# Performance work log

Measured on AMD Instinct MI355X. Metric: run time of the kernel, lower is better.

Reference implementation:

```python
import jax, jax.numpy as jnp
import numpy as np

N = 50000   # nodes
E = 800000  # edges
F = 64      # node_feature_dim
H = 128     # hidden_dim


def setup_inputs() -> dict:
    key = jax.random.key(0)
    ks = jax.random.split(key, 20)
    def w(k, shape, fan_in):
        return jax.random.normal(k, shape, jnp.float32) / np.sqrt(fan_in)
    return {
        "x": jax.random.normal(ks[0], (N, F), jnp.float32),
        "edge_index": jax.random.randint(ks[1], (2, E), 0, N, jnp.int32),
        "enc_w1": w(ks[2], (F, H), F), "enc_b1": jnp.zeros((H,), jnp.float32),
        "enc_w2": w(ks[3], (H, H), H), "enc_b2": jnp.zeros((H,), jnp.float32),
        "w_c1": w(ks[4], (H, H), H), "b_c1": jnp.zeros((H,), jnp.float32),
        "w_c2": w(ks[5], (H, H), H), "b_c2": jnp.zeros((H,), jnp.float32),
        "w_c3": w(ks[6], (H, H), H), "b_c3": jnp.zeros((H,), jnp.float32),
        "dec_w1": w(ks[7], (H, H), H), "dec_b1": jnp.zeros((H,), jnp.float32),
        "dec_w2": w(ks[8], (H, F), H), "dec_b2": jnp.zeros((F,), jnp.float32),
    }


def _gcn_conv(h, W, b, src, dst, dinv):
    # PyG GCNConv: D^-1/2 (A+I) D^-1/2 (h W) + b  (self-loops already in src/dst)
    hw = h @ W                                   # [N, H]
    norm = dinv[src] * dinv[dst]                 # [E+N]
    msg = hw[src] * norm[:, None]                # gather + scale
    return jax.ops.segment_sum(msg, dst, num_segments=N) + b


def reference(x, edge_index, enc_w1, enc_b1, enc_w2, enc_b2,
              w_c1, b_c1, w_c2, b_c2, w_c3, b_c3,
              dec_w1, dec_b1, dec_w2, dec_b2):
    loop = jnp.arange(N, dtype=edge_index.dtype)
    src = jnp.concatenate([edge_index[0], loop])
    dst = jnp.concatenate([edge_index[1], loop])
    deg = jax.ops.segment_sum(jnp.ones_like(dst, jnp.float32), dst, num_segments=N)
    dinv = jax.lax.rsqrt(deg)  # deg >= 1 because of self-loops

    h = jax.nn.relu(x @ enc_w1 + enc_b1) @ enc_w2 + enc_b2  # encoder MLP
    h = jax.nn.relu(_gcn_conv(h, w_c1, b_c1, src, dst, dinv))
    h = jax.nn.relu(_gcn_conv(h, w_c2, b_c2, src, dst, dinv))
    h = jax.nn.relu(_gcn_conv(h, w_c3, b_c3, src, dst, dinv))
    # window_size == 1: chunk+cat is identity
    out = jax.nn.relu(h @ dec_w1 + dec_b1) @ dec_w2 + dec_b2  # decoder MLP
    return jax.nn.sigmoid(out)
```

## Files before the change

kernel.cpp:

```cpp
#include <hip/hip_runtime.h>
#include <stdint.h>

#define NN 50000
#define NE 800000
#define FD 64
#define HD 128
#define NBKT 196
#define BCAP 5120
#define P1E 8192

typedef __attribute__((ext_vector_type(8))) short short8;
typedef __attribute__((ext_vector_type(4))) float f32x4;

#define AS1 __attribute__((address_space(1)))
#define AS3 __attribute__((address_space(3)))

__device__ __forceinline__ float bflo(unsigned int v) {
    union { unsigned int u; float f; } c; c.u = v << 16; return c.f;
}
__device__ __forceinline__ float bfhi(unsigned int v) {
    union { unsigned int u; float f; } c; c.u = v & 0xffff0000u; return c.f;
}
__device__ __forceinline__ unsigned short f2bf(float f) {
    union { float f; unsigned int u; } c; c.f = f;
    unsigned int u = c.u;
    return (unsigned short)((u + 0x7fffu + ((u >> 16) & 1u)) >> 16);
}
__device__ __forceinline__ unsigned int pack2(float a, float b) {
    return (unsigned int)f2bf(a) | ((unsigned int)f2bf(b) << 16);
}

__global__ void wt0_k(const float* __restrict__ w0, unsigned short* __restrict__ t0) {
    int e = blockIdx.x * 256 + threadIdx.x;
    int k = e >> 7, c = e & 127;
    int gsw = (k >> 3) ^ (c & 7);
    t0[c * 64 + gsw * 8 + (k & 7)] = f2bf(w0[e]);
}

template <int K, int COLS, int EPI, bool BIAS, bool RSCALE, bool A_F32, bool OUT_F32>
__device__ __forceinline__ void mgemm_dev(
    int bid,
    const void* __restrict__ Av,
    const unsigned short* __restrict__ Wt,
    const float* __restrict__ bias,
    const float* __restrict__ dinv,
    void* __restrict__ outv, int nrows)
{
    constexpr int NB = COLS / 16;
    constexpr int KC = K / 32;
    constexpr int GMASK = (K >> 3) - 1;
    __shared__ __align__(16) unsigned char Ws8[COLS * K * 2];

    const int tid = threadIdx.x;
    const int wave = tid >> 6;
    const int lane = tid & 63;

    {
        constexpr int ROUNDS = COLS * K * 2 / 4096;
        const int gb = wave * 1024 + lane * 16;
        const int lb = wave * 1024;
        #pragma unroll
        for (int r = 0; r < ROUNDS; r++) {
            __builtin_amdgcn_global_load_lds(
                (const AS1 unsigned int*)((const unsigned char*)Wt + r * 4096 + gb),
                (AS3 unsigned int*)(Ws8 + r * 4096 + lb),
                16, 0, 0);
        }
    }

    const int m = lane & 15;
    const int q = lane >> 4;
    const int row0 = bid * 64 + wave * 16;

    f32x4 acc[NB];
    #pragma unroll
    for (int i = 0; i < NB; i++) acc[i] = (f32x4){0.f, 0.f, 0.f, 0.f};

    const bool arow_ok = !A_F32 || (row0 + m) < nrows;

    short8 af[KC];
    #pragma unroll
    for (int kc = 0; kc < KC; kc++) {
        if constexpr (A_F32) {
            const float* arowf = (const float*)Av + (size_t)(row0 + m) * K + q * 8 + kc * 32;
            float4 lo = make_float4(0.f, 0.f, 0.f, 0.f), hi = lo;
            if (arow_ok) { lo = *(const float4*)arowf; hi = *(const float4*)(arowf + 4); }
            af[kc][0] = (short)f2bf(lo.x); af[kc][1] = (short)f2bf(lo.y);
            af[kc][2] = (short)f2bf(lo.z); af[kc][3] = (short)f2bf(lo.w);
            af[kc][4] = (short)f2bf(hi.x); af[kc][5] = (short)f2bf(hi.y);
            af[kc][6] = (short)f2bf(hi.z); af[kc][7] = (short)f2bf(hi.w);
        } else {
            const unsigned short* arow = (const unsigned short*)Av + (size_t)(row0 + m) * K + q * 8 + kc * 32;
            af[kc] = *(const short8*)arow;
        }
    }
    __syncthreads();

    #pragma unroll
    for (int kc = 0; kc < KC; kc++) {
        #pragma unroll
        for (int nb = 0; nb < NB; nb++) {
            const int c = nb * 16 + m;
            const int gsw = (kc * 4 + q) ^ (c & GMASK);
            short8 bf = *(const short8*)&Ws8[(c * K + gsw * 8) * 2];
            acc[nb] = __builtin_amdgcn_mfma_f32_16x16x32_bf16(af[kc], bf, acc[nb], 0, 0, 0);
        }
    }

    float bv[NB];
    #pragma unroll
    for (int nb = 0; nb < NB; nb++) bv[nb] = BIAS ? bias[nb * 16 + m] : 0.f;

    #pragma unroll
    for (int r = 0; r < 4; r++) {
        int row = row0 + q * 4 + r;
        if (row < nrows) {
            float sc = RSCALE ? dinv[row] : 1.f;
            #pragma unroll
            for (int nb = 0; nb < NB; nb++) {
                float t = acc[nb][r];
                if (RSCALE) t *= sc;
                t += bv[nb];
                if (EPI == 1) t = fmaxf(t, 0.f);
                if (EPI == 2) t = 1.f / (1.f + __expf(-t));
                if constexpr (OUT_F32) {
                    ((float*)outv)[(size_t)row * COLS + nb * 16 + m] = t;
                } else {
                    ((unsigned short*)outv)[(size_t)row * COLS + nb * 16 + m] = f2bf(t);
                }
            }
        }
    }
}

template <int K, int COLS, int EPI, bool BIAS, bool RSCALE, bool A_F32, bool OUT_F32>
__global__ __launch_bounds__(256) void mgemm_k(
    const void* __restrict__ Av, const unsigned short* __restrict__ Wt,
    const float* __restrict__ bias, const float* __restrict__ dinv,
    void* __restrict__ outv, int nrows)
{
    mgemm_dev<K, COLS, EPI, BIAS, RSCALE, A_F32, OUT_F32>(blockIdx.x, Av, Wt, bias, dinv, outv, nrows);
}

__global__ __launch_bounds__(256) void k1_k(
    const float* __restrict__ x, const unsigned short* __restrict__ t0s,
    const float* __restrict__ enc_b1, unsigned short* __restrict__ bufA,
    const int* __restrict__ src, const int* __restrict__ dst,
    int* __restrict__ gcnt, unsigned int* __restrict__ bucket,
    const float* __restrict__ w1, const float* __restrict__ w2,
    const float* __restrict__ w3, const float* __restrict__ w4,
    const float* __restrict__ w5, const float* __restrict__ w6,
    unsigned short* __restrict__ t1, unsigned short* __restrict__ t2,
    unsigned short* __restrict__ t3, unsigned short* __restrict__ t4,
    unsigned short* __restrict__ t5, unsigned short* __restrict__ t6,
    int gb, int pb)
{
    const int b = blockIdx.x;
    if (b < gb) {
        mgemm_dev<64, 128, 1, true, false, true, false>(b, x, t0s, enc_b1, nullptr, bufA, NN);
    } else if (b < gb + pb) {
        __shared__ int lcnt[256], lsw[256], lexc[256], lofs[256], lrank[256];
        __shared__ unsigned int stage[P1E];
        const int tid = threadIdx.x;
        const int bb = b - gb;
        lcnt[tid] = 0; lrank[tid] = 0;
        __syncthreads();
        unsigned int ent[P1E / 256];
        #pragma unroll
        for (int u = 0; u < P1E / 256; u++) {
            int g = bb * P1E + u * 256 + tid;
            if (g < NE) {
                int d = dst[g], s = src[g];
                int bk = d >> 8;
                atomicAdd(&lcnt[bk], 1);
                ent[u] = (unsigned int)s | ((unsigned int)(d & 255) << 16)
                       | ((unsigned int)bk << 24);
            } else ent[u] = 0xFFFFFFFFu;
        }
        __syncthreads();
        int v = lcnt[tid];
        lsw[tid] = v; __syncthreads();
        for (int d = 1; d < 256; d <<= 1) {
            int xx = (tid >= d) ? lsw[tid - d] : 0; __syncthreads();
            lsw[tid] += xx; __syncthreads();
        }
        lexc[tid] = lsw[tid] - v;
        lofs[tid] = (v > 0) ? atomicAdd(&gcnt[tid], v) : 0;
        __syncthreads();
        #pragma unroll
        for (int u = 0; u < P1E / 256; u++) {
            if (ent[u] != 0xFFFFFFFFu) {
                int bk = ent[u] >> 24;
                int r = atomicAdd(&lrank[bk], 1);
                stage[lexc[bk] + r] = ent[u];
            }
        }
        __syncthreads();
        int cb = NE - bb * P1E; if (cb > P1E) cb = P1E;
        for (int i = tid; i < cb; i += 256) {
            unsigned int e = stage[i];
            int bk = e >> 24;
            bucket[(size_t)bk * BCAP + lofs[bk] + (i - lexc[bk])] = e;
        }
    } else {
        int b2 = b - gb - pb;
        const float* W; unsigned short* T; int C = 128;
        if      (b2 <  64) { W = w1; T = t1; }
        else if (b2 < 128) { W = w2; T = t2; b2 -= 64; }
        else if (b2 < 192) { W = w3; T = t3; b2 -= 128; }
        else if (b2 < 256) { W = w4; T = t4; b2 -= 192; }
        else if (b2 < 320) { W = w5; T = t5; b2 -= 256; }
        else               { W = w6; T = t6; b2 -= 320; C = 64; }
        int e = b2 * 256 + threadIdx.x;
        int k, c;
        if (C == 128) { k = e >> 7; c = e & 127; } else { k = e >> 6; c = e & 63; }
        int gsw = (k >> 3) ^ (c & 15);
        T[c * 128 + gsw * 8 + (k & 7)] = f2bf(W[e]);
    }
}

__global__ __launch_bounds__(256) void k2_k(
    const unsigned short* __restrict__ bufA, const unsigned short* __restrict__ t1,
    const float* __restrict__ enc_b2, unsigned short* __restrict__ bufB,
    const int* __restrict__ gcnt, const unsigned int* __restrict__ bucket,
    int* __restrict__ off, float* __restrict__ dinv,
    unsigned short* __restrict__ csr, int gb)
{
    if ((int)blockIdx.x < gb) {
        mgemm_dev<128, 128, 0, true, false, false, false>(blockIdx.x, bufA, t1, enc_b2, nullptr, bufB, NN);
    } else {
        __shared__ int lc[256], sw[256], sexc[256], lr[256], gsh[256];
        const int tid = threadIdx.x;
        const int b = blockIdx.x - gb;
        int gv = (tid < NBKT) ? gcnt[tid] : 0;
        gsh[tid] = gv; __syncthreads();
        for (int d = 1; d < 256; d <<= 1) {
            int xx = (tid >= d) ? gsh[tid - d] : 0; __syncthreads();
            gsh[tid] += xx; __syncthreads();
        }
        const int cb = gcnt[b];
        const int base = gsh[b] - cb;
        unsigned int ent[BCAP / 256];
        #pragma unroll
        for (int u = 0; u < BCAP / 256; u++) {
            int i = u * 256 + tid;
            ent[u] = (i < cb) ? bucket[(size_t)b * BCAP + i] : 0xFFFFFFFFu;
        }
        lc[tid] = 0; lr[tid] = 0;
        __syncthreads();
        #pragma unroll
        for (int u = 0; u < BCAP / 256; u++)
            if (ent[u] != 0xFFFFFFFFu) atomicAdd(&lc[(ent[u] >> 16) & 255], 1);
        __syncthreads();
        int v = lc[tid];
        int node = b * 256 + tid;
        if (node < NN) dinv[node] = rsqrtf((float)(v + 1));
        sw[tid] = v; __syncthreads();
        for (int d = 1; d < 256; d <<= 1) {
            int xx = (tid >= d) ? sw[tid - d] : 0; __syncthreads();
            sw[tid] += xx; __syncthreads();
        }
        sexc[tid] = sw[tid] - v;
        if (node < NN) off[node] = base + sexc[tid];
        if (b == NBKT - 1 && tid == 0) off[NN] = NE;
        __syncthreads();
        #pragma unroll
        for (int u = 0; u < BCAP / 256; u++) {
            if (ent[u] != 0xFFFFFFFFu) {
                int dl = (ent[u] >> 16) & 255;
                int r = atomicAdd(&lr[dl], 1);
                csr[base + sexc[dl] + r] = (unsigned short)(ent[u] & 0xffff);
            }
        }
    }
}

__global__ __launch_bounds__(256) void agg_k(
    const uint2* __restrict__ hws,
    const int* __restrict__ off,
    const unsigned short* __restrict__ csr,
    const float* __restrict__ dinv, const float* __restrict__ bias,
    uint2* __restrict__ out, int n)
{
    int node = blockIdx.x * 8 + (threadIdx.x >> 5);
    if (node >= n) return;
    int lane = threadIdx.x & 31;

    uint2 v = hws[node * 32 + lane];
    float s0 = bflo(v.x), s1 = bfhi(v.x), s2 = bflo(v.y), s3 = bfhi(v.y);

    int b = off[node], e = off[node + 1];
    int j = b;
    for (; j + 8 <= e; j += 8) {
        uint2 t[8];
        #pragma unroll
        for (int u = 0; u < 8; u++) t[u] = hws[(int)csr[j + u] * 32 + lane];
        #pragma unroll
        for (int u = 0; u < 8; u++) {
            s0 += bflo(t[u].x); s1 += bfhi(t[u].x);
            s2 += bflo(t[u].y); s3 += bfhi(t[u].y);
        }
    }
    for (; j < e; j++) {
        uint2 t = hws[(int)csr[j] * 32 + lane];
        s0 += bflo(t.x); s1 += bfhi(t.x);
        s2 += bflo(t.y); s3 += bfhi(t.y);
    }

    float di = dinv[node];
    float4 bv = *(const float4*)(bias + 4 * lane);
    float r0 = fmaxf(fmaf(di, s0, bv.x), 0.f);
    float r1 = fmaxf(fmaf(di, s1, bv.y), 0.f);
    float r2 = fmaxf(fmaf(di, s2, bv.z), 0.f);
    float r3 = fmaxf(fmaf(di, s3, bv.w), 0.f);
    uint2 o; o.x = pack2(r0, r1); o.y = pack2(r2, r3);
    out[node * 32 + lane] = o;
}

extern "C" void kernel_launch(void* const* d_in, const int* in_sizes, int n_in,
                              void* d_out, int out_size, void* d_ws, size_t ws_size,
                              hipStream_t stream)
{
    const float* x      = (const float*)d_in[0];
    const int*   ei     = (const int*)d_in[1];
    const float* enc_w1 = (const float*)d_in[2];
    const float* enc_b1 = (const float*)d_in[3];
    const float* enc_w2 = (const float*)d_in[4];
    const float* enc_b2 = (const float*)d_in[5];
    const float* w_c1   = (const float*)d_in[6];
    const float* b_c1   = (const float*)d_in[7];
    const float* w_c2   = (const float*)d_in[8];
    const float* b_c2   = (const float*)d_in[9];
    const float* w_c3   = (const float*)d_in[10];
    const float* b_c3   = (const float*)d_in[11];
    const float* dec_w1 = (const float*)d_in[12];
    const float* dec_b1 = (const float*)d_in[13];
    const float* dec_w2 = (const float*)d_in[14];
    const float* dec_b2 = (const float*)d_in[15];

    const int* src = ei;
    const int* dst = ei + NE;

    const int NP = 50048;

    char* ws = (char*)d_ws;
    size_t o = 0;
    auto alloc = [&](size_t bytes) -> void* {
        void* p = ws + o;
        o = (o + bytes + 255) & ~(size_t)255;
        return p;
    };
    int*   gcnt = (int*)alloc(256 * 4);
    int*   off  = (int*)alloc((size_t)(NN + 1) * 4);
    unsigned short* csr = (unsigned short*)alloc((size_t)NE * 2);
    unsigned int* bucket = (unsigned int*)alloc((size_t)NBKT * BCAP * 4);
    float* dinv = (float*)alloc((size_t)NN * 4);
    unsigned short* bufA = (unsigned short*)alloc((size_t)NP * HD * 2);
    unsigned short* bufB = (unsigned short*)alloc((size_t)NP * HD * 2);
    unsigned short* t0 = (unsigned short*)alloc(64 * 128 * 2);
    unsigned short* t1 = (unsigned short*)alloc(128 * 128 * 2);
    unsigned short* t2 = (unsigned short*)alloc(128 * 128 * 2);
    unsigned short* t3 = (unsigned short*)alloc(128 * 128 * 2);
    unsigned short* t4 = (unsigned short*)alloc(128 * 128 * 2);
    unsigned short* t5 = (unsigned short*)alloc(128 * 128 * 2);
    unsigned short* t6 = (unsigned short*)alloc(128 * 64 * 2);
    (void)ws_size; (void)n_in; (void)in_sizes; (void)out_size;

    hipMemsetAsync(gcnt, 0, 256 * 4, stream);

    const int PB = (NE + P1E - 1) / P1E;
    const int GB = NP / 64;
    const int AB = (NN + 7) / 8;

    wt0_k<<<32, 256, 0, stream>>>(enc_w1, t0);
    k1_k<<<GB + PB + 352, 256, 0, stream>>>(x, t0, enc_b1, bufA, src, dst, gcnt, bucket,
                                            enc_w2, w_c1, w_c2, w_c3, dec_w1, dec_w2,
                                            t1, t2, t3, t4, t5, t6, GB, PB);
    k2_k<<<GB + NBKT, 256, 0, stream>>>(bufA, t1, enc_b2, bufB, gcnt, bucket,
                                        off, dinv, csr, GB);
    mgemm_k<128, 128, 0, false, true, false, false><<<GB, 256, 0, stream>>>(bufB, t2, nullptr, dinv, bufA, NN);
    agg_k<<<AB, 256, 0, stream>>>((const uint2*)bufA, off, csr, dinv, b_c1, (uint2*)bufB, NN);
    mgemm_k<128, 128, 0, false, true, false, false><<<GB, 256, 0, stream>>>(bufB, t3, nullptr, dinv, bufA, NN);
    agg_k<<<AB, 256, 0, stream>>>((const uint2*)bufA, off, csr, dinv, b_c2, (uint2*)bufB, NN);
    mgemm_k<128, 128, 0, false, true, false, false><<<GB, 256, 0, stream>>>(bufB, t4, nullptr, dinv, bufA, NN);
    agg_k<<<AB, 256, 0, stream>>>((const uint2*)bufA, off, csr, dinv, b_c3, (uint2*)bufB, NN);
    mgemm_k<128, 128, 1, true, false, false, false><<<GB, 256, 0, stream>>>(bufB, t5, dec_b1, nullptr, bufA, NN);
    mgemm_k<128, 64, 2, true, false, false, true><<<GB, 256, 0, stream>>>(bufA, t6, dec_b2, nullptr, d_out, NN);
}
```

Before: 283.8 us.

## Fuse GCN aggregation with next-layer GEMM and decoder MLP into single kernels

```diff
diff --git a/kernel.cpp b/kernel.cpp
--- a/kernel.cpp
+++ b/kernel.cpp
@@ -275,46 +275,281 @@
     }
 }
 
-__global__ __launch_bounds__(256) void agg_k(
-    const uint2* __restrict__ hws,
-    const int* __restrict__ off,
-    const unsigned short* __restrict__ csr,
-    const float* __restrict__ dinv, const float* __restrict__ bias,
-    uint2* __restrict__ out, int n)
+__global__ __launch_bounds__(256) void aggm_k(
+    const uint4* __restrict__ hws, const int* __restrict__ off,
+    const unsigned short* __restrict__ csr, const float* __restrict__ dinv,
+    const float* __restrict__ bias, const unsigned short* __restrict__ Wt,
+    unsigned short* __restrict__ out, int n)
 {
-    int node = blockIdx.x * 8 + (threadIdx.x >> 5);
-    if (node >= n) return;
-    int lane = threadIdx.x & 31;
-
-    uint2 v = hws[node * 32 + lane];
-    float s0 = bflo(v.x), s1 = bfhi(v.x), s2 = bflo(v.y), s3 = bfhi(v.y);
-
-    int b = off[node], e = off[node + 1];
-    int j = b;
-    for (; j + 8 <= e; j += 8) {
-        uint2 t[8];
-        #pragma unroll
-        for (int u = 0; u < 8; u++) t[u] = hws[(int)csr[j + u] * 32 + lane];
-        #pragma unroll
-        for (int u = 0; u < 8; u++) {
-            s0 += bflo(t[u].x); s1 += bfhi(t[u].x);
-            s2 += bflo(t[u].y); s3 += bfhi(t[u].y);
-        }
-    }
-    for (; j < e; j++) {
-        uint2 t = hws[(int)csr[j] * 32 + lane];
-        s0 += bflo(t.x); s1 += bfhi(t.x);
-        s2 += bflo(t.y); s3 += bfhi(t.y);
-    }
-
-    float di = dinv[node];
-    float4 bv = *(const float4*)(bias + 4 * lane);
-    float r0 = fmaxf(fmaf(di, s0, bv.x), 0.f);
-    float r1 = fmaxf(fmaf(di, s1, bv.y), 0.f);
-    float r2 = fmaxf(fmaf(di, s2, bv.z), 0.f);
-    float r3 = fmaxf(fmaf(di, s3, bv.w), 0.f);
-    uint2 o; o.x = pack2(r0, r1); o.y = pack2(r2, r3);
-    out[node * 32 + lane] = o;
+    __shared__ __align__(16) unsigned char sm[49152];
+    unsigned char* Ws8 = sm;
+    uint4* g4 = (uint4*)(sm + 32768);
+
+    const int tid = threadIdx.x;
+    const int wave = tid >> 6;
+    const int lane = tid & 63;
+    const int bid = blockIdx.x;
+
+    {
+        const int gb = wave * 1024 + lane * 16;
+        const int lb = wave * 1024;
+        #pragma unroll
+        for (int r = 0; r < 8; r++)
+            __builtin_amdgcn_global_load_lds(
+                (const AS1 unsigned int*)((const unsigned char*)Wt + r * 4096 + gb),
+                (AS3 unsigned int*)(Ws8 + r * 4096 + lb), 16, 0, 0);
+    }
+
+    const int g16 = tid >> 4;
+    const int l16 = tid & 15;
+    const float4 b0 = *(const float4*)(bias + 8 * l16);
+    const float4 b1 = *(const float4*)(bias + 8 * l16 + 4);
+
+    #pragma unroll
+    for (int it = 0; it < 4; it++) {
+        const int ri = it * 16 + g16;
+        const int row = bid * 64 + ri;
+        if (row < n) {
+            uint4 v = hws[(size_t)row * 16 + l16];
+            float s0 = bflo(v.x), s1 = bfhi(v.x), s2 = bflo(v.y), s3 = bfhi(v.y);
+            float s4 = bflo(v.z), s5 = bfhi(v.z), s6 = bflo(v.w), s7 = bfhi(v.w);
+            const int je = off[row + 1];
+            int j = off[row];
+            for (; j + 8 <= je; j += 8) {
+                uint4 t[8];
+                #pragma unroll
+                for (int u = 0; u < 8; u++) t[u] = hws[(size_t)csr[j + u] * 16 + l16];
+                #pragma unroll
+                for (int u = 0; u < 8; u++) {
+                    s0 += bflo(t[u].x); s1 += bfhi(t[u].x);
+                    s2 += bflo(t[u].y); s3 += bfhi(t[u].y);
+                    s4 += bflo(t[u].z); s5 += bfhi(t[u].z);
+                    s6 += bflo(t[u].w); s7 += bfhi(t[u].w);
+                }
+            }
+            for (; j < je; j++) {
+                uint4 t = hws[(size_t)csr[j] * 16 + l16];
+                s0 += bflo(t.x); s1 += bfhi(t.x);
+                s2 += bflo(t.y); s3 += bfhi(t.y);
+                s4 += bflo(t.z); s5 += bfhi(t.z);
+                s6 += bflo(t.w); s7 += bfhi(t.w);
+            }
+            const float di = dinv[row];
+            uint4 o;
+            o.x = pack2(fmaxf(fmaf(di, s0, b0.x), 0.f), fmaxf(fmaf(di, s1, b0.y), 0.f));
+            o.y = pack2(fmaxf(fmaf(di, s2, b0.z), 0.f), fmaxf(fmaf(di, s3, b0.w), 0.f));
+            o.z = pack2(fmaxf(fmaf(di, s4, b1.x), 0.f), fmaxf(fmaf(di, s5, b1.y), 0.f));
+            o.w = pack2(fmaxf(fmaf(di, s6, b1.z), 0.f), fmaxf(fmaf(di, s7, b1.w), 0.f));
+            g4[ri * 16 + (l16 ^ g16)] = o;
+        }
+    }
+    __syncthreads();
+
+    const int m = lane & 15;
+    const int q = lane >> 4;
+
+    short8 af[4];
+    #pragma unroll
+    for (int kc = 0; kc < 4; kc++)
+        af[kc] = *(const short8*)&g4[(wave * 16 + m) * 16 + ((q + kc * 4) ^ m)];
+
+    f32x4 acc[8];
+    #pragma unroll
+    for (int i = 0; i < 8; i++) acc[i] = (f32x4){0.f, 0.f, 0.f, 0.f};
+
+    #pragma unroll
+    for (int kc = 0; kc < 4; kc++) {
+        #pragma unroll
+        for (int nb = 0; nb < 8; nb++) {
+            const int c = nb * 16 + m;
+            const int gsw = (kc * 4 + q) ^ (c & 15);
+            short8 bf = *(const short8*)&Ws8[(c * 128 + gsw * 8) * 2];
+            acc[nb] = __builtin_amdgcn_mfma_f32_16x16x32_bf16(af[kc], bf, acc[nb], 0, 0, 0);
+        }
+    }
+
+    const int row0 = bid * 64 + wave * 16;
+    #pragma unroll
+    for (int r = 0; r < 4; r++) {
+        const int row = row0 + q * 4 + r;
+        if (row < n) {
+            const float sc = dinv[row];
+            #pragma unroll
+            for (int nb = 0; nb < 8; nb++)
+                out[(size_t)row * 128 + nb * 16 + m] = f2bf(acc[nb][r] * sc);
+        }
+    }
+}
+
+__global__ __launch_bounds__(256) void dec_k(
+    const uint4* __restrict__ hws, const int* __restrict__ off,
+    const unsigned short* __restrict__ csr, const float* __restrict__ dinv,
+    const float* __restrict__ bias,
+    const unsigned short* __restrict__ Wt1, const float* __restrict__ db1,
+    const unsigned short* __restrict__ Wt2, const float* __restrict__ db2,
+    float* __restrict__ outp, int n)
+{
+    __shared__ __align__(16) unsigned char sm[49152];
+    unsigned char* Ws8 = sm;
+    uint4* g4 = (uint4*)(sm + 32768);
+
+    const int tid = threadIdx.x;
+    const int wave = tid >> 6;
+    const int lane = tid & 63;
+    const int bid = blockIdx.x;
+
+    {
+        const int gb = wave * 1024 + lane * 16;
+        const int lb = wave * 1024;
+        #pragma unroll
+        for (int r = 0; r < 8; r++)
+            __builtin_amdgcn_global_load_lds(
+                (const AS1 unsigned int*)((const unsigned char*)Wt1 + r * 4096 + gb),
+                (AS3 unsigned int*)(Ws8 + r * 4096 + lb), 16, 0, 0);
+    }
+
+    {
+        const int g16 = tid >> 4;
+        const int l16 = tid & 15;
+        const float4 b0 = *(const float4*)(bias + 8 * l16);
+        const float4 b1 = *(const float4*)(bias + 8 * l16 + 4);
+        #pragma unroll
+        for (int it = 0; it < 4; it++) {
+            const int ri = it * 16 + g16;
+            const int row = bid * 64 + ri;
+            if (row < n) {
+                uint4 v = hws[(size_t)row * 16 + l16];
+                float s0 = bflo(v.x), s1 = bfhi(v.x), s2 = bflo(v.y), s3 = bfhi(v.y);
+                float s4 = bflo(v.z), s5 = bfhi(v.z), s6 = bflo(v.w), s7 = bfhi(v.w);
+                const int je = off[row + 1];
+                int j = off[row];
+                for (; j + 8 <= je; j += 8) {
+                    uint4 t[8];
+                    #pragma unroll
+                    for (int u = 0; u < 8; u++) t[u] = hws[(size_t)csr[j + u] * 16 + l16];
+                    #pragma unroll
+                    for (int u = 0; u < 8; u++) {
+                        s0 += bflo(t[u].x); s1 += bfhi(t[u].x);
+                        s2 += bflo(t[u].y); s3 += bfhi(t[u].y);
+                        s4 += bflo(t[u].z); s5 += bfhi(t[u].z);
+                        s6 += bflo(t[u].w); s7 += bfhi(t[u].w);
+                    }
+                }
+                for (; j < je; j++) {
+                    uint4 t = hws[(size_t)csr[j] * 16 + l16];
+                    s0 += bflo(t.x); s1 += bfhi(t.x);
+                    s2 += bflo(t.y); s3 += bfhi(t.y);
+                    s4 += bflo(t.z); s5 += bfhi(t.z);
+                    s6 += bflo(t.w); s7 += bfhi(t.w);
+                }
+                const float di = dinv[row];
+                uint4 o;
+                o.x = pack2(fmaxf(fmaf(di, s0, b0.x), 0.f), fmaxf(fmaf(di, s1, b0.y), 0.f));
+                o.y = pack2(fmaxf(fmaf(di, s2, b0.z), 0.f), fmaxf(fmaf(di, s3, b0.w), 0.f));
+                o.z = pack2(fmaxf(fmaf(di, s4, b1.x), 0.f), fmaxf(fmaf(di, s5, b1.y), 0.f));
+                o.w = pack2(fmaxf(fmaf(di, s6, b1.z), 0.f), fmaxf(fmaf(di, s7, b1.w), 0.f));
+                g4[ri * 16 + (l16 ^ g16)] = o;
+            }
+        }
+    }
+    __syncthreads();
+
+    const int m = lane & 15;
+    const int q = lane >> 4;
+
+    f32x4 at0[4], at1[4];
+    #pragma unroll
+    for (int i = 0; i < 4; i++) { at0[i] = (f32x4){0.f,0.f,0.f,0.f}; at1[i] = at0[i]; }
+
+    #pragma unroll
+    for (int kc = 0; kc < 4; kc++) {
+        short8 wf0, wf1, gf[4];
+        {
+            const int c0 = (wave * 2 + 0) * 16 + m;
+            const int c1 = (wave * 2 + 1) * 16 + m;
+            wf0 = *(const short8*)&Ws8[(c0 * 128 + (((kc * 4 + q) ^ (c0 & 15)) * 8)) * 2];
+            wf1 = *(const short8*)&Ws8[(c1 * 128 + (((kc * 4 + q) ^ (c1 & 15)) * 8)) * 2];
+        }
+        #pragma unroll
+        for (int nt = 0; nt < 4; nt++)
+            gf[nt] = *(const short8*)&g4[(nt * 16 + m) * 16 + ((q + kc * 4) ^ m)];
+        #pragma unroll
+        for (int nt = 0; nt < 4; nt++) {
+            at0[nt] = __builtin_amdgcn_mfma_f32_16x16x32_bf16(wf0, gf[nt], at0[nt], 0, 0, 0);
+            at1[nt] = __builtin_amdgcn_mfma_f32_16x16x32_bf16(wf1, gf[nt], at1[nt], 0, 0, 0);
+        }
+    }
+    __syncthreads();
+
+    {
+        const int gb = wave * 1024 + lane * 16;
+        const int lb = wave * 1024;
+        #pragma unroll
+        for (int r = 0; r < 4; r++)
+            __builtin_amdgcn_global_load_lds(
+                (const AS1 unsigned int*)((const unsigned char*)Wt2 + r * 4096 + gb),
+                (AS3 unsigned int*)(Ws8 + r * 4096 + lb), 16, 0, 0);
+    }
+
+    {
+        uint2* g2 = (uint2*)g4;
+        #pragma unroll
+        for (int f2 = 0; f2 < 2; f2++) {
+            const int ftile = wave * 2 + f2;
+            const float4 bb = *(const float4*)(db1 + ftile * 16 + q * 4);
+            const int G = ftile * 2 + (q >> 1);
+            #pragma unroll
+            for (int nt = 0; nt < 4; nt++) {
+                const int row = nt * 16 + m;
+                const f32x4 a = f2 ? at1[nt] : at0[nt];
+                float v0 = fmaxf(a[0] + bb.x, 0.f);
+                float v1 = fmaxf(a[1] + bb.y, 0.f);
+                float v2 = fmaxf(a[2] + bb.z, 0.f);
+                float v3 = fmaxf(a[3] + bb.w, 0.f);
+                uint2 hv; hv.x = pack2(v0, v1); hv.y = pack2(v2, v3);
+                g2[row * 32 + (((G ^ (row & 15)) << 1) | (q & 1))] = hv;
+            }
+        }
+    }
+    __syncthreads();
+
+    short8 af[4];
+    #pragma unroll
+    for (int kc = 0; kc < 4; kc++)
+        af[kc] = *(const short8*)&g4[(wave * 16 + m) * 16 + ((q + kc * 4) ^ m)];
+
+    f32x4 a2[4];
+    #pragma unroll
+    for (int i = 0; i < 4; i++) a2[i] = (f32x4){0.f, 0.f, 0.f, 0.f};
+
+    #pragma unroll
+    for (int kc = 0; kc < 4; kc++) {
+        #pragma unroll
+        for (int nb = 0; nb < 4; nb++) {
+            const int c = nb * 16 + m;
+            const int gsw = (kc * 4 + q) ^ (c & 15);
+            short8 bf = *(const short8*)&Ws8[(c * 128 + gsw * 8) * 2];
+            a2[nb] = __builtin_amdgcn_mfma_f32_16x16x32_bf16(af[kc], bf, a2[nb], 0, 0, 0);
+        }
+    }
+
+    float bv[4];
+    #pragma unroll
+    for (int nb = 0; nb < 4; nb++) bv[nb] = db2[nb * 16 + m];
+
+    const int row0 = bid * 64 + wave * 16;
+    #pragma unroll
+    for (int r = 0; r < 4; r++) {
+        const int row = row0 + q * 4 + r;
+        if (row < n) {
+            #pragma unroll
+            for (int nb = 0; nb < 4; nb++) {
+                float t = a2[nb][r] + bv[nb];
+                t = 1.f / (1.f + __expf(-t));
+                outp[(size_t)row * 64 + nb * 16 + m] = t;
+            }
+        }
+    }
 }
 
 extern "C" void kernel_launch(void* const* d_in, const int* in_sizes, int n_in,
@@ -370,7 +605,6 @@
 
     const int PB = (NE + P1E - 1) / P1E;
     const int GB = NP / 64;
-    const int AB = (NN + 7) / 8;
 
     wt0_k<<<32, 256, 0, stream>>>(enc_w1, t0);
     k1_k<<<GB + PB + 352, 256, 0, stream>>>(x, t0, enc_b1, bufA, src, dst, gcnt, bucket,
@@ -379,11 +613,8 @@
     k2_k<<<GB + NBKT, 256, 0, stream>>>(bufA, t1, enc_b2, bufB, gcnt, bucket,
                                         off, dinv, csr, GB);
     mgemm_k<128, 128, 0, false, true, false, false><<<GB, 256, 0, stream>>>(bufB, t2, nullptr, dinv, bufA, NN);
-    agg_k<<<AB, 256, 0, stream>>>((const uint2*)bufA, off, csr, dinv, b_c1, (uint2*)bufB, NN);
-    mgemm_k<128, 128, 0, false, true, false, false><<<GB, 256, 0, stream>>>(bufB, t3, nullptr, dinv, bufA, NN);
-    agg_k<<<AB, 256, 0, stream>>>((const uint2*)bufA, off, csr, dinv, b_c2, (uint2*)bufB, NN);
-    mgemm_k<128, 128, 0, false, true, false, false><<<GB, 256, 0, stream>>>(bufB, t4, nullptr, dinv, bufA, NN);
-    agg_k<<<AB, 256, 0, stream>>>((const uint2*)bufA, off, csr, dinv, b_c3, (uint2*)bufB, NN);
-    mgemm_k<128, 128, 1, true, false, false, false><<<GB, 256, 0, stream>>>(bufB, t5, dec_b1, nullptr, bufA, NN);
-    mgemm_k<128, 64, 2, true, false, false, true><<<GB, 256, 0, stream>>>(bufA, t6, dec_b2, nullptr, d_out, NN);
-}
+    aggm_k<<<GB, 256, 0, stream>>>((const uint4*)bufA, off, csr, dinv, b_c1, t3, bufB, NN);
+    aggm_k<<<GB, 256, 0, stream>>>((const uint4*)bufB, off, csr, dinv, b_c2, t4, bufA, NN);
+    dec_k<<<GB, 256, 0, stream>>>((const uint4*)bufA, off, csr, dinv, b_c3,
+                                  t5, dec_b1, t6, dec_b2, (float*)d_out, NN);
+}
```

Result: slower. 310.3 us (+9.3%).

## Fuse GCN aggregation with following 128x128 GEMM in per-16-row kernel

Applied to the files above, without the earlier changes.

```diff
diff --git a/kernel.cpp b/kernel.cpp
--- a/kernel.cpp
+++ b/kernel.cpp
@@ -8,6 +8,8 @@
 #define NBKT 196
 #define BCAP 5120
 #define P1E 8192
+
+static_assert(NN % 16 == 0, "aggm16 grid is exact");
 
 typedef __attribute__((ext_vector_type(8))) short short8;
 typedef __attribute__((ext_vector_type(4))) float f32x4;
@@ -275,46 +277,98 @@
     }
 }
 
-__global__ __launch_bounds__(256) void agg_k(
-    const uint2* __restrict__ hws,
-    const int* __restrict__ off,
-    const unsigned short* __restrict__ csr,
-    const float* __restrict__ dinv, const float* __restrict__ bias,
-    uint2* __restrict__ out, int n)
-{
-    int node = blockIdx.x * 8 + (threadIdx.x >> 5);
-    if (node >= n) return;
-    int lane = threadIdx.x & 31;
-
-    uint2 v = hws[node * 32 + lane];
-    float s0 = bflo(v.x), s1 = bfhi(v.x), s2 = bflo(v.y), s3 = bfhi(v.y);
-
-    int b = off[node], e = off[node + 1];
-    int j = b;
-    for (; j + 8 <= e; j += 8) {
-        uint2 t[8];
-        #pragma unroll
-        for (int u = 0; u < 8; u++) t[u] = hws[(int)csr[j + u] * 32 + lane];
-        #pragma unroll
-        for (int u = 0; u < 8; u++) {
-            s0 += bflo(t[u].x); s1 += bfhi(t[u].x);
-            s2 += bflo(t[u].y); s3 += bfhi(t[u].y);
-        }
-    }
-    for (; j < e; j++) {
-        uint2 t = hws[(int)csr[j] * 32 + lane];
-        s0 += bflo(t.x); s1 += bfhi(t.x);
-        s2 += bflo(t.y); s3 += bfhi(t.y);
-    }
-
-    float di = dinv[node];
-    float4 bv = *(const float4*)(bias + 4 * lane);
-    float r0 = fmaxf(fmaf(di, s0, bv.x), 0.f);
-    float r1 = fmaxf(fmaf(di, s1, bv.y), 0.f);
-    float r2 = fmaxf(fmaf(di, s2, bv.z), 0.f);
-    float r3 = fmaxf(fmaf(di, s3, bv.w), 0.f);
-    uint2 o; o.x = pack2(r0, r1); o.y = pack2(r2, r3);
-    out[node * 32 + lane] = o;
+template <int EPI, bool BIAS, bool RSCALE>
+__global__ __launch_bounds__(256) void aggm16_k(
+    const uint4* __restrict__ hws, const int* __restrict__ off,
+    const unsigned short* __restrict__ csr, const float* __restrict__ dinv,
+    const float* __restrict__ gbias,
+    const unsigned short* __restrict__ Wt,
+    const float* __restrict__ obias,
+    unsigned short* __restrict__ out)
+{
+    __shared__ __align__(16) uint4 g4[16 * 16];
+
+    const int tid = threadIdx.x;
+    const int bid = blockIdx.x;
+    const int wave = tid >> 6;
+    const int lane = tid & 63;
+    const int m = lane & 15;
+    const int q = lane >> 4;
+
+    short8 Bf0[4], Bf1[4];
+    #pragma unroll
+    for (int kc = 0; kc < 4; kc++) {
+        const int c0 = wave * 32 + m;
+        const int c1 = c0 + 16;
+        Bf0[kc] = *(const short8*)&Wt[c0 * 128 + (((kc * 4 + q) ^ (c0 & 15)) << 3)];
+        Bf1[kc] = *(const short8*)&Wt[c1 * 128 + (((kc * 4 + q) ^ (c1 & 15)) << 3)];
+    }
+
+    {
+        const int g = tid >> 4;
+        const int l = tid & 15;
+        const int row = bid * 16 + g;
+        const float4 b0 = *(const float4*)(gbias + 8 * l);
+        const float4 b1 = *(const float4*)(gbias + 8 * l + 4);
+
+        uint4 v = hws[(size_t)row * 16 + l];
+        float s0 = bflo(v.x), s1 = bfhi(v.x), s2 = bflo(v.y), s3 = bfhi(v.y);
+        float s4 = bflo(v.z), s5 = bfhi(v.z), s6 = bflo(v.w), s7 = bfhi(v.w);
+        const int je = off[row + 1];
+        int j = off[row];
+        for (; j + 8 <= je; j += 8) {
+            uint4 t[8];
+            #pragma unroll
+            for (int u = 0; u < 8; u++) t[u] = hws[(size_t)csr[j + u] * 16 + l];
+            #pragma unroll
+            for (int u = 0; u < 8; u++) {
+                s0 += bflo(t[u].x); s1 += bfhi(t[u].x);
+                s2 += bflo(t[u].y); s3 += bfhi(t[u].y);
+                s4 += bflo(t[u].z); s5 += bfhi(t[u].z);
+                s6 += bflo(t[u].w); s7 += bfhi(t[u].w);
+            }
+        }
+        for (; j < je; j++) {
+            uint4 t = hws[(size_t)csr[j] * 16 + l];
+            s0 += bflo(t.x); s1 += bfhi(t.x);
+            s2 += bflo(t.y); s3 += bfhi(t.y);
+            s4 += bflo(t.z); s5 += bfhi(t.z);
+            s6 += bflo(t.w); s7 += bfhi(t.w);
+        }
+        const float di = dinv[row];
+        uint4 o;
+        o.x = pack2(fmaxf(fmaf(di, s0, b0.x), 0.f), fmaxf(fmaf(di, s1, b0.y), 0.f));
+        o.y = pack2(fmaxf(fmaf(di, s2, b0.z), 0.f), fmaxf(fmaf(di, s3, b0.w), 0.f));
+        o.z = pack2(fmaxf(fmaf(di, s4, b1.x), 0.f), fmaxf(fmaf(di, s5, b1.y), 0.f));
+        o.w = pack2(fmaxf(fmaf(di, s6, b1.z), 0.f), fmaxf(fmaf(di, s7, b1.w), 0.f));
+        g4[g * 16 + (l ^ g)] = o;
+    }
+    __syncthreads();
+
+    f32x4 a0 = (f32x4){0.f, 0.f, 0.f, 0.f}, a1 = a0;
+    #pragma unroll
+    for (int kc = 0; kc < 4; kc++) {
+        short8 af = *(const short8*)&g4[m * 16 + ((q + kc * 4) ^ m)];
+        a0 = __builtin_amdgcn_mfma_f32_16x16x32_bf16(af, Bf0[kc], a0, 0, 0, 0);
+        a1 = __builtin_amdgcn_mfma_f32_16x16x32_bf16(af, Bf1[kc], a1, 0, 0, 0);
+    }
+
+    const int c0 = wave * 32 + m;
+    const int c1 = c0 + 16;
+    const float bv0 = BIAS ? obias[c0] : 0.f;
+    const float bv1 = BIAS ? obias[c1] : 0.f;
+
+    #pragma unroll
+    for (int r = 0; r < 4; r++) {
+        const int row = bid * 16 + q * 4 + r;
+        const float sc = RSCALE ? dinv[row] : 1.f;
+        float t0 = a0[r], t1 = a1[r];
+        if (RSCALE) { t0 *= sc; t1 *= sc; }
+        t0 += bv0; t1 += bv1;
+        if (EPI == 1) { t0 = fmaxf(t0, 0.f); t1 = fmaxf(t1, 0.f); }
+        out[(size_t)row * 128 + c0] = f2bf(t0);
+        out[(size_t)row * 128 + c1] = f2bf(t1);
+    }
 }
 
 extern "C" void kernel_launch(void* const* d_in, const int* in_sizes, int n_in,
@@ -368,9 +422,9 @@
 
     hipMemsetAsync(gcnt, 0, 256 * 4, stream);
 
-    const int PB = (NE + P1E - 1) / P1E;
-    const int GB = NP / 64;
-    const int AB = (NN + 7) / 8;
+    const int PB   = (NE + P1E - 1) / P1E;
+    const int GB   = NP / 64;
+    const int GB16 = NN / 16;
 
     wt0_k<<<32, 256, 0, stream>>>(enc_w1, t0);
     k1_k<<<GB + PB + 352, 256, 0, stream>>>(x, t0, enc_b1, bufA, src, dst, gcnt, bucket,
@@ -379,11 +433,8 @@
     k2_k<<<GB + NBKT, 256, 0, stream>>>(bufA, t1, enc_b2, bufB, gcnt, bucket,
                                         off, dinv, csr, GB);
     mgemm_k<128, 128, 0, false, true, false, false><<<GB, 256, 0, stream>>>(bufB, t2, nullptr, dinv, bufA, NN);
-    agg_k<<<AB, 256, 0, stream>>>((const uint2*)bufA, off, csr, dinv, b_c1, (uint2*)bufB, NN);
-    mgemm_k<128, 128, 0, false, true, false, false><<<GB, 256, 0, stream>>>(bufB, t3, nullptr, dinv, bufA, NN);
-    agg_k<<<AB, 256, 0, stream>>>((const uint2*)bufA, off, csr, dinv, b_c2, (uint2*)bufB, NN);
-    mgemm_k<128, 128, 0, false, true, false, false><<<GB, 256, 0, stream>>>(bufB, t4, nullptr, dinv, bufA, NN);
-    agg_k<<<AB, 256, 0, stream>>>((const uint2*)bufA, off, csr, dinv, b_c3, (uint2*)bufB, NN);
-    mgemm_k<128, 128, 1, true, false, false, false><<<GB, 256, 0, stream>>>(bufB, t5, dec_b1, nullptr, bufA, NN);
-    mgemm_k<128, 64, 2, true, false, false, true><<<GB, 256, 0, stream>>>(bufA, t6, dec_b2, nullptr, d_out, NN);
-}
+    aggm16_k<0, false, true><<<GB16, 256, 0, stream>>>((const uint4*)bufA, off, csr, dinv, b_c1, t3, nullptr, bufB);
+    aggm16_k<0, false, true><<<GB16, 256, 0, stream>>>((const uint4*)bufB, off, csr, dinv, b_c2, t4, nullptr, bufA);
+    aggm16_k<1, true, false><<<GB16, 256, 0, stream>>>((const uint4*)bufA, off, csr, dinv, b_c3, t5, dec_b1, bufB);
+    mgemm_k<128, 64, 2, true, false, false, true><<<GB, 256, 0, stream>>>(bufB, t6, dec_b2, nullptr, d_out, NN);
+}
```

Result: faster. 277.9 us (-2.1%).
